# Kernel optimization log

Hardware: AMD Instinct MI355X
Metric: run time of the kernel (lower is better)

The kernel has to match this reference:

```python
import jax, jax.numpy as jnp
import numpy as np
import math

B, S, D = 8, 2048, 1024

def setup_inputs() -> dict:
    key = jax.random.key(0)
    ks = jax.random.split(key, 9)
    scale = 1.0 / math.sqrt(D)
    Q = jax.random.normal(ks[0], (B, S, D), dtype=jnp.float32)
    K = jax.random.normal(ks[1], (B, S, D), dtype=jnp.float32)
    V = jax.random.normal(ks[2], (B, S, D), dtype=jnp.float32)
    Wq = jax.random.normal(ks[3], (D, D), dtype=jnp.float32) * scale
    Wk = jax.random.normal(ks[4], (D, D), dtype=jnp.float32) * scale
    Wv = jax.random.normal(ks[5], (D, D), dtype=jnp.float32) * scale
    bq = jnp.zeros((D,), dtype=jnp.float32)
    bk = jnp.zeros((D,), dtype=jnp.float32)
    bv = jnp.zeros((D,), dtype=jnp.float32)
    # causal mask, broadcast over batch: [1, S, S]
    mask = jnp.tril(jnp.ones((S, S), dtype=jnp.int32))[None, :, :]
    return {"Q": Q, "K": K, "V": V, "Wq": Wq, "Wk": Wk, "Wv": Wv,
            "bq": bq, "bk": bk, "bv": bv, "mask": mask}

def reference(Q, K, V, Wq, Wk, Wv, bq, bk, bv, mask):
    d_model = Q.shape[-1]
    q = jnp.einsum('bsd,de->bse', Q, Wq) + bq
    k = jnp.einsum('bsd,de->bse', K, Wk) + bk
    v = jnp.einsum('bsd,de->bse', V, Wv) + bv
    scores = jnp.einsum('bqd,bkd->bqk', q, k) / math.sqrt(d_model)  # [B,S,S]
    scores = jnp.where(mask == 0, jnp.float32(-1e9), scores)
    weights = jax.nn.softmax(scores, axis=-1)
    out = jnp.einsum('bqk,bkd->bqd', weights, v)
    return out
```

## Files before the change

kernel.cpp:

```cpp
#include <hip/hip_runtime.h>
#include <hip/hip_bf16.h>

#define Bb 8
#define Ss 2048
#define Dd 1024

typedef short bf16x8 __attribute__((ext_vector_type(8)));
typedef float f32x4  __attribute__((ext_vector_type(4)));

__device__ __forceinline__ short f2bf(float f) {
  union { __hip_bfloat16 h; short s; } u;
  u.h = __float2bfloat16(f);
  return u.s;
}
__device__ __forceinline__ float bf2f(short s) {
  union { unsigned int u; float f; } v;
  v.u = ((unsigned int)(unsigned short)s) << 16;
  return v.f;
}

__device__ __forceinline__ int swz(int row, int slot) {
  return row * 64 + (((slot ^ row) & 7) << 3);
}
__device__ __forceinline__ int swzf(int row, int slot) {
  return row * 64 + (((slot ^ row) & 15) << 2);
}

__device__ __forceinline__ void stage_glds(const short* __restrict__ src, int ld,
                                           short* lds, int tid) {
  int w = tid >> 6;
#pragma unroll
  for (int it = 0; it < 4; ++it) {
    int u = it * 256 + tid;
    int r = u >> 3;
    int ssrc = (u ^ r) & 7;
    const short* g = src + (size_t)r * ld + ssrc * 8;
    short* lbase = lds + (size_t)(it * 256 + w * 64) * 8;
    __builtin_amdgcn_global_load_lds((const __attribute__((address_space(1))) void*)g,
                                     (__attribute__((address_space(3))) void*)lbase,
                                     16, 0, 0);
  }
}

__device__ __forceinline__ void stage_glds_f32(const float* __restrict__ src, int ld,
                                               float* lds, int tid) {
  int w = tid >> 6;
#pragma unroll
  for (int it = 0; it < 8; ++it) {
    int u = it * 256 + tid;
    int r = u >> 4;
    int ssrc = (u ^ r) & 15;
    const float* g = src + (size_t)r * ld + ssrc * 4;
    float* lbase = lds + (size_t)(it * 256 + w * 64) * 4;
    __builtin_amdgcn_global_load_lds((const __attribute__((address_space(1))) void*)g,
                                     (__attribute__((address_space(3))) void*)lbase,
                                     16, 0, 0);
  }
}

__device__ __forceinline__ void mfma_tile(const short* ldsA, const short* ldsB,
                                          f32x4 acc[4][4], int wm, int wn, int lr, int lk) {
#pragma unroll
  for (int c = 0; c < 2; ++c) {
    bf16x8 afr[4], bfr[4];
#pragma unroll
    for (int m = 0; m < 4; ++m)
      afr[m] = *(const bf16x8*)&ldsA[swz(wm * 64 + m * 16 + lr, c * 4 + lk)];
#pragma unroll
    for (int n = 0; n < 4; ++n)
      bfr[n] = *(const bf16x8*)&ldsB[swz(wn * 64 + n * 16 + lr, c * 4 + lk)];
#pragma unroll
    for (int m = 0; m < 4; ++m)
#pragma unroll
      for (int n = 0; n < 4; ++n)
        acc[m][n] = __builtin_amdgcn_mfma_f32_16x16x32_bf16(afr[m], bfr[n], acc[m][n], 0, 0, 0);
  }
}

__device__ __forceinline__ void mfma_tile_f32A(const float* ldsA, const short* ldsB,
                                               f32x4 acc[4][4], int wm, int wn,
                                               int lr, int lk) {
#pragma unroll
  for (int c = 0; c < 2; ++c) {
    bf16x8 afr[4], bfr[4];
#pragma unroll
    for (int m = 0; m < 4; ++m) {
      int r = wm * 64 + m * 16 + lr;
      int s0 = c * 8 + lk * 2;
      f32x4 a0 = *(const f32x4*)&ldsA[swzf(r, s0)];
      f32x4 a1 = *(const f32x4*)&ldsA[swzf(r, s0 + 1)];
      bf16x8 h;
      h[0] = f2bf(a0[0]); h[1] = f2bf(a0[1]); h[2] = f2bf(a0[2]); h[3] = f2bf(a0[3]);
      h[4] = f2bf(a1[0]); h[5] = f2bf(a1[1]); h[6] = f2bf(a1[2]); h[7] = f2bf(a1[3]);
      afr[m] = h;
    }
#pragma unroll
    for (int n = 0; n < 4; ++n)
      bfr[n] = *(const bf16x8*)&ldsB[swz(wn * 64 + n * 16 + lr, c * 4 + lk)];
#pragma unroll
    for (int m = 0; m < 4; ++m)
#pragma unroll
      for (int n = 0; n < 4; ++n)
        acc[m][n] = __builtin_amdgcn_mfma_f32_16x16x32_bf16(afr[m], bfr[n], acc[m][n], 0, 0, 0);
  }
}

__global__ void wcast_kernel(const float* __restrict__ Wq, const float* __restrict__ Wk,
                             const float* __restrict__ Wv,
                             short* __restrict__ WtQ, short* __restrict__ WtK,
                             short* __restrict__ WtV) {
  int z = blockIdx.z;
  const float* W = (z == 0) ? Wq : (z == 1) ? Wk : Wv;
  short* Wt      = (z == 0) ? WtQ : (z == 1) ? WtK : WtV;
  __shared__ float tile[32][33];
  int r0 = blockIdx.y * 32, c0 = blockIdx.x * 32;
  int tx = threadIdx.x, ty = threadIdx.y;
#pragma unroll
  for (int ii = 0; ii < 4; ++ii) {
    int r = ty * 4 + ii;
    tile[r][tx] = W[(size_t)(r0 + r) * Dd + c0 + tx];
  }
  __syncthreads();
#pragma unroll
  for (int ii = 0; ii < 4; ++ii) {
    int c = ty * 4 + ii;
    Wt[(size_t)(c0 + c) * Dd + r0 + tx] = f2bf(tile[tx][c]);
  }
}

__launch_bounds__(256, 3)
__global__ void proj_kernel(const float* __restrict__ Q, const float* __restrict__ Kin,
                            const float* __restrict__ V,
                            const short* __restrict__ WtQ, const short* __restrict__ WtK,
                            const short* __restrict__ WtV,
                            const float* __restrict__ bq, const float* __restrict__ bk,
                            const float* __restrict__ bv,
                            short* __restrict__ qb, short* __restrict__ kb,
                            short* __restrict__ vT) {
  __shared__ float ldsA[128 * 64];
  __shared__ short ldsB[128 * 64];
  int z = blockIdx.y;
  const float* A    = (z == 0) ? Q : (z == 1) ? Kin : V;
  const short* W    = (z == 0) ? WtQ : (z == 1) ? WtK : WtV;
  const float* bias = (z == 0) ? bq : (z == 1) ? bk : bv;

  int r = blockIdx.x;
  int x = r & 7;
  int s = r >> 3;
  int nblk = s & 7;
  int mblk = x + 8 * (s >> 3);
  int m0 = mblk * 128;
  int n0 = nblk * 128;

  int tid = threadIdx.x;
  int lane = tid & 63, w = tid >> 6;
  int wm = w >> 1, wn = w & 1;
  int lr = lane & 15, lk = lane >> 4;

  const float* Ab = A + (size_t)m0 * Dd;
  const short* Wb = W + (size_t)n0 * Dd;

  f32x4 acc[4][4] = {};
  for (int k0 = 0; k0 < Dd; k0 += 64) {
    __syncthreads();
    stage_glds_f32(Ab + k0, Dd, ldsA, tid);
    stage_glds(Wb + k0, Dd, ldsB, tid);
    __syncthreads();
    mfma_tile_f32A(ldsA, ldsB, acc, wm, wn, lr, lk);
  }

  if (z < 2) {
    short* out = (z == 0) ? qb : kb;
#pragma unroll
    for (int m = 0; m < 4; ++m)
#pragma unroll
      for (int n = 0; n < 4; ++n) {
        int col = n0 + wn * 64 + n * 16 + lr;
        float bv_ = bias[col];
        int rbase = m0 + wm * 64 + m * 16 + lk * 4;
#pragma unroll
        for (int rr = 0; rr < 4; ++rr)
          out[(size_t)(rbase + rr) * Dd + col] = f2bf(acc[m][n][rr] + bv_);
      }
  } else {
#pragma unroll
    for (int m = 0; m < 4; ++m)
#pragma unroll
      for (int n = 0; n < 4; ++n) {
        int col = n0 + wn * 64 + n * 16 + lr;
        float bv_ = bias[col];
        int rbase = m0 + wm * 64 + m * 16 + lk * 4;
        int bidx = rbase / Ss;
        int s0 = rbase & (Ss - 1);
        short4 h;
        h.x = f2bf(acc[m][n][0] + bv_);
        h.y = f2bf(acc[m][n][1] + bv_);
        h.z = f2bf(acc[m][n][2] + bv_);
        h.w = f2bf(acc[m][n][3] + bv_);
        *(short4*)&vT[(size_t)bidx * Dd * Ss + (size_t)col * Ss + s0] = h;
      }
  }
}

__launch_bounds__(256, 4)
__global__ void score_kernel(const short* __restrict__ qb, const short* __restrict__ kb,
                             short* __restrict__ SP) {
  int d = blockIdx.x;
  int b = d & 7;
  int sidx = d >> 3;
  int i = (int)((sqrtf(8.f * sidx + 1.f) - 1.f) * 0.5f);
  while ((i + 1) * (i + 2) / 2 <= sidx) ++i;
  while (i * (i + 1) / 2 > sidx) --i;
  int j = sidx - i * (i + 1) / 2;

  __shared__ short ldsA[128 * 64];
  __shared__ short ldsB[128 * 64];
  int tid = threadIdx.x;
  int lane = tid & 63, w = tid >> 6;
  int wm = w >> 1, wn = w & 1;
  int lr = lane & 15, lk = lane >> 4;

  const short* Abase = qb + (size_t)b * Ss * Dd + (size_t)i * 128 * Dd;
  const short* Bbase = kb + (size_t)b * Ss * Dd + (size_t)j * 128 * Dd;

  f32x4 acc[4][4] = {};
  for (int k0 = 0; k0 < Dd; k0 += 64) {
    __syncthreads();
    stage_glds(Abase + k0, Dd, ldsA, tid);
    stage_glds(Bbase + k0, Dd, ldsB, tid);
    __syncthreads();
    mfma_tile(ldsA, ldsB, acc, wm, wn, lr, lk);
  }

  short* srow = SP + (size_t)b * Ss * Ss;
#pragma unroll
  for (int m = 0; m < 4; ++m)
#pragma unroll
    for (int n = 0; n < 4; ++n) {
      int colg = j * 128 + wn * 64 + n * 16 + lr;
      int rbase = i * 128 + wm * 64 + m * 16 + lk * 4;
#pragma unroll
      for (int rr = 0; rr < 4; ++rr) {
        int rowg = rbase + rr;
        float sv = acc[m][n][rr] * 0.03125f;
        if (colg > rowg) sv = -1e9f;
        srow[(size_t)rowg * Ss + colg] = f2bf(sv);
      }
    }
}

__global__ void softmax_kernel(short* __restrict__ SP) {
  int row = blockIdx.x;
  int b = row >> 11;
  int q = row & (Ss - 1);
  int L = ((q >> 7) + 1) << 7;
  short* srow = SP + (size_t)b * Ss * Ss + (size_t)q * Ss;
  int tid = threadIdx.x;
  int lane = tid & 63, w = tid >> 6;

  float vals[8];
  int cnt = 0;
  float mx = -3.0e38f;
  for (int c = tid; c < L; c += 256) {
    float f = bf2f(srow[c]);
    vals[cnt++] = f;
    mx = fmaxf(mx, f);
  }
  __shared__ float red[8];
#pragma unroll
  for (int off = 32; off; off >>= 1) mx = fmaxf(mx, __shfl_xor(mx, off));
  if (lane == 0) red[w] = mx;
  __syncthreads();
  mx = fmaxf(fmaxf(red[0], red[1]), fmaxf(red[2], red[3]));

  float sum = 0.f;
  for (int k2 = 0; k2 < cnt; ++k2) {
    float e = __expf(vals[k2] - mx);
    vals[k2] = e;
    sum += e;
  }
#pragma unroll
  for (int off = 32; off; off >>= 1) sum += __shfl_xor(sum, off);
  if (lane == 0) red[4 + w] = sum;
  __syncthreads();
  sum = red[4] + red[5] + red[6] + red[7];
  float inv = 1.0f / sum;

  cnt = 0;
  for (int c = tid; c < L; c += 256) srow[c] = f2bf(vals[cnt++] * inv);
}

__launch_bounds__(256, 4)
__global__ void pv_kernel(const short* __restrict__ SP, const short* __restrict__ vT,
                          float* __restrict__ out) {
  int d = blockIdx.x;
  int b = d & 7;
  int s = d >> 3;
  int i = s >> 3;
  int dblk = s & 7;

  __shared__ short ldsA[128 * 64];
  __shared__ short ldsB[128 * 64];
  int tid = threadIdx.x;
  int lane = tid & 63, w = tid >> 6;
  int wm = w >> 1, wn = w & 1;
  int lr = lane & 15, lk = lane >> 4;

  const short* Abase = SP + (size_t)b * Ss * Ss + (size_t)i * 128 * Ss;
  const short* Bbase = vT + (size_t)b * Dd * Ss + (size_t)dblk * 128 * Ss;
  int KL = (i + 1) * 128;

  f32x4 acc[4][4] = {};
  for (int k0 = 0; k0 < KL; k0 += 64) {
    __syncthreads();
    stage_glds(Abase + k0, Ss, ldsA, tid);
    stage_glds(Bbase + k0, Ss, ldsB, tid);
    __syncthreads();
    mfma_tile(ldsA, ldsB, acc, wm, wn, lr, lk);
  }

#pragma unroll
  for (int m = 0; m < 4; ++m)
#pragma unroll
    for (int n = 0; n < 4; ++n) {
      int colg = dblk * 128 + wn * 64 + n * 16 + lr;
      int rbase = i * 128 + wm * 64 + m * 16 + lk * 4;
#pragma unroll
      for (int rr = 0; rr < 4; ++rr)
        out[(size_t)b * Ss * Dd + (size_t)(rbase + rr) * Dd + colg] = acc[m][n][rr];
    }
}

extern "C" void kernel_launch(void* const* d_in, const int* in_sizes, int n_in,
                              void* d_out, int out_size, void* d_ws, size_t ws_size,
                              hipStream_t stream) {
  const float* Q  = (const float*)d_in[0];
  const float* K  = (const float*)d_in[1];
  const float* V  = (const float*)d_in[2];
  const float* Wq = (const float*)d_in[3];
  const float* Wk = (const float*)d_in[4];
  const float* Wv = (const float*)d_in[5];
  const float* bq = (const float*)d_in[6];
  const float* bk = (const float*)d_in[7];
  const float* bv = (const float*)d_in[8];
  float* out = (float*)d_out;

  char* ws = (char*)d_ws;
  size_t off = 0;
  short* WtQ = (short*)(ws + off); off += (size_t)Dd * Dd * 2;
  short* WtK = (short*)(ws + off); off += (size_t)Dd * Dd * 2;
  short* WtV = (short*)(ws + off); off += (size_t)Dd * Dd * 2;
  short* qb  = (short*)(ws + off); off += (size_t)Bb * Ss * Dd * 2;
  short* kb  = (short*)(ws + off); off += (size_t)Bb * Ss * Dd * 2;
  short* vT  = (short*)(ws + off); off += (size_t)Bb * Ss * Dd * 2;
  short* SP  = (short*)(ws + off); off += (size_t)Bb * Ss * Ss * 2;
  (void)ws_size; (void)in_sizes; (void)n_in; (void)out_size;

  wcast_kernel<<<dim3(32, 32, 3), dim3(32, 8), 0, stream>>>(Wq, Wk, Wv, WtQ, WtK, WtV);
  proj_kernel<<<dim3(1024, 3), 256, 0, stream>>>(Q, K, V, WtQ, WtK, WtV, bq, bk, bv,
                                                 qb, kb, vT);
  score_kernel<<<dim3(1088), 256, 0, stream>>>(qb, kb, SP);
  softmax_kernel<<<dim3(Bb * Ss), 256, 0, stream>>>(SP);
  pv_kernel<<<dim3(1024), 256, 0, stream>>>(SP, vT, out);
}
```

Before: 313.0 us.

## Halve projection K-tile for higher occupancy and vectorize softmax row access

The projection GEMM now stages K-chunks of 32 instead of 64. This shrinks the fp32 A tile and the bf16 B tile in LDS, uses new swizzle layouts, and raises launch bounds from 3 to 6 blocks per CU to increase occupancy. The trade-off is twice as many barrier-separated loop iterations and less MFMA work per sync. The softmax kernel also switches from strided scalar bf16 loads and stores to one 16-byte vector per thread, which reduces memory instructions.

```diff
diff --git a/kernel.cpp b/kernel.cpp
--- a/kernel.cpp
+++ b/kernel.cpp
@@ -22,8 +22,18 @@
 __device__ __forceinline__ int swz(int row, int slot) {
   return row * 64 + (((slot ^ row) & 7) << 3);
 }
-__device__ __forceinline__ int swzf(int row, int slot) {
-  return row * 64 + (((slot ^ row) & 15) << 2);
+__device__ __forceinline__ int swzA32(int row, int slot) {
+  return row * 32 + (((slot ^ row) & 7) << 2);
+}
+__device__ __forceinline__ int swzp(int r, int lk) {
+  int R = r >> 1;
+  int slot = ((r & 1) << 2) | lk;
+  return R * 64 + (((slot ^ R) & 7) << 3);
+}
+
+__device__ __forceinline__ void gld16(const void* g, void* l) {
+  __builtin_amdgcn_global_load_lds((const __attribute__((address_space(1))) void*)g,
+                                   (__attribute__((address_space(3))) void*)l, 16, 0, 0);
 }
 
 __device__ __forceinline__ void stage_glds(const short* __restrict__ src, int ld,
@@ -34,27 +44,34 @@
     int u = it * 256 + tid;
     int r = u >> 3;
     int ssrc = (u ^ r) & 7;
-    const short* g = src + (size_t)r * ld + ssrc * 8;
-    short* lbase = lds + (size_t)(it * 256 + w * 64) * 8;
-    __builtin_amdgcn_global_load_lds((const __attribute__((address_space(1))) void*)g,
-                                     (__attribute__((address_space(3))) void*)lbase,
-                                     16, 0, 0);
-  }
-}
-
-__device__ __forceinline__ void stage_glds_f32(const float* __restrict__ src, int ld,
-                                               float* lds, int tid) {
+    gld16(src + (size_t)r * ld + ssrc * 8, lds + (size_t)(it * 256 + w * 64) * 8);
+  }
+}
+
+__device__ __forceinline__ void stage_A32(const float* __restrict__ src, int ld,
+                                          float* lds, int tid) {
   int w = tid >> 6;
 #pragma unroll
-  for (int it = 0; it < 8; ++it) {
+  for (int it = 0; it < 4; ++it) {
     int u = it * 256 + tid;
-    int r = u >> 4;
-    int ssrc = (u ^ r) & 15;
-    const float* g = src + (size_t)r * ld + ssrc * 4;
-    float* lbase = lds + (size_t)(it * 256 + w * 64) * 4;
-    __builtin_amdgcn_global_load_lds((const __attribute__((address_space(1))) void*)g,
-                                     (__attribute__((address_space(3))) void*)lbase,
-                                     16, 0, 0);
+    int r = u >> 3;
+    int sl = u & 7;
+    int s = sl ^ (r & 7);
+    gld16(src + (size_t)r * ld + s * 4, lds + (size_t)(it * 256 + w * 64) * 4);
+  }
+}
+
+__device__ __forceinline__ void stage_B32(const short* __restrict__ src, int ld,
+                                          short* lds, int tid) {
+  int w = tid >> 6;
+#pragma unroll
+  for (int it = 0; it < 2; ++it) {
+    int u = it * 256 + tid;
+    int R = u >> 3, sl = u & 7;
+    int pre = sl ^ (R & 7);
+    int r = (R << 1) | (pre >> 2);
+    int kc = pre & 3;
+    gld16(src + (size_t)r * ld + kc * 8, lds + (size_t)(it * 256 + w * 64) * 8);
   }
 }
 
@@ -66,34 +83,6 @@
 #pragma unroll
     for (int m = 0; m < 4; ++m)
       afr[m] = *(const bf16x8*)&ldsA[swz(wm * 64 + m * 16 + lr, c * 4 + lk)];
-#pragma unroll
-    for (int n = 0; n < 4; ++n)
-      bfr[n] = *(const bf16x8*)&ldsB[swz(wn * 64 + n * 16 + lr, c * 4 + lk)];
-#pragma unroll
-    for (int m = 0; m < 4; ++m)
-#pragma unroll
-      for (int n = 0; n < 4; ++n)
-        acc[m][n] = __builtin_amdgcn_mfma_f32_16x16x32_bf16(afr[m], bfr[n], acc[m][n], 0, 0, 0);
-  }
-}
-
-__device__ __forceinline__ void mfma_tile_f32A(const float* ldsA, const short* ldsB,
-                                               f32x4 acc[4][4], int wm, int wn,
-                                               int lr, int lk) {
-#pragma unroll
-  for (int c = 0; c < 2; ++c) {
-    bf16x8 afr[4], bfr[4];
-#pragma unroll
-    for (int m = 0; m < 4; ++m) {
-      int r = wm * 64 + m * 16 + lr;
-      int s0 = c * 8 + lk * 2;
-      f32x4 a0 = *(const f32x4*)&ldsA[swzf(r, s0)];
-      f32x4 a1 = *(const f32x4*)&ldsA[swzf(r, s0 + 1)];
-      bf16x8 h;
-      h[0] = f2bf(a0[0]); h[1] = f2bf(a0[1]); h[2] = f2bf(a0[2]); h[3] = f2bf(a0[3]);
-      h[4] = f2bf(a1[0]); h[5] = f2bf(a1[1]); h[6] = f2bf(a1[2]); h[7] = f2bf(a1[3]);
-      afr[m] = h;
-    }
 #pragma unroll
     for (int n = 0; n < 4; ++n)
       bfr[n] = *(const bf16x8*)&ldsB[swz(wn * 64 + n * 16 + lr, c * 4 + lk)];
@@ -128,7 +117,7 @@
   }
 }
 
-__launch_bounds__(256, 3)
+__launch_bounds__(256, 6)
 __global__ void proj_kernel(const float* __restrict__ Q, const float* __restrict__ Kin,
                             const float* __restrict__ V,
                             const short* __restrict__ WtQ, const short* __restrict__ WtK,
@@ -137,8 +126,8 @@
                             const float* __restrict__ bv,
                             short* __restrict__ qb, short* __restrict__ kb,
                             short* __restrict__ vT) {
-  __shared__ float ldsA[128 * 64];
-  __shared__ short ldsB[128 * 64];
+  __shared__ float ldsA[128 * 32];
+  __shared__ short ldsB[64 * 64];
   int z = blockIdx.y;
   const float* A    = (z == 0) ? Q : (z == 1) ? Kin : V;
   const short* W    = (z == 0) ? WtQ : (z == 1) ? WtK : WtV;
@@ -161,12 +150,30 @@
   const short* Wb = W + (size_t)n0 * Dd;
 
   f32x4 acc[4][4] = {};
-  for (int k0 = 0; k0 < Dd; k0 += 64) {
-    __syncthreads();
-    stage_glds_f32(Ab + k0, Dd, ldsA, tid);
-    stage_glds(Wb + k0, Dd, ldsB, tid);
-    __syncthreads();
-    mfma_tile_f32A(ldsA, ldsB, acc, wm, wn, lr, lk);
+  for (int k0 = 0; k0 < Dd; k0 += 32) {
+    __syncthreads();
+    stage_A32(Ab + k0, Dd, ldsA, tid);
+    stage_B32(Wb + k0, Dd, ldsB, tid);
+    __syncthreads();
+    bf16x8 afr[4], bfr[4];
+#pragma unroll
+    for (int m = 0; m < 4; ++m) {
+      int rr = wm * 64 + m * 16 + lr;
+      f32x4 a0 = *(const f32x4*)&ldsA[swzA32(rr, lk * 2)];
+      f32x4 a1 = *(const f32x4*)&ldsA[swzA32(rr, lk * 2 + 1)];
+      bf16x8 h;
+      h[0] = f2bf(a0[0]); h[1] = f2bf(a0[1]); h[2] = f2bf(a0[2]); h[3] = f2bf(a0[3]);
+      h[4] = f2bf(a1[0]); h[5] = f2bf(a1[1]); h[6] = f2bf(a1[2]); h[7] = f2bf(a1[3]);
+      afr[m] = h;
+    }
+#pragma unroll
+    for (int n = 0; n < 4; ++n)
+      bfr[n] = *(const bf16x8*)&ldsB[swzp(wn * 64 + n * 16 + lr, lk)];
+#pragma unroll
+    for (int m = 0; m < 4; ++m)
+#pragma unroll
+      for (int n = 0; n < 4; ++n)
+        acc[m][n] = __builtin_amdgcn_mfma_f32_16x16x32_bf16(afr[m], bfr[n], acc[m][n], 0, 0, 0);
   }
 
   if (z < 2) {
@@ -257,14 +264,18 @@
   short* srow = SP + (size_t)b * Ss * Ss + (size_t)q * Ss;
   int tid = threadIdx.x;
   int lane = tid & 63, w = tid >> 6;
-
-  float vals[8];
-  int cnt = 0;
+  int c8 = tid * 8;
+  bool act = c8 < L;
+
+  float v[8];
   float mx = -3.0e38f;
-  for (int c = tid; c < L; c += 256) {
-    float f = bf2f(srow[c]);
-    vals[cnt++] = f;
-    mx = fmaxf(mx, f);
+  if (act) {
+    bf16x8 hv = *(const bf16x8*)&srow[c8];
+#pragma unroll
+    for (int j2 = 0; j2 < 8; ++j2) {
+      v[j2] = bf2f(hv[j2]);
+      mx = fmaxf(mx, v[j2]);
+    }
   }
   __shared__ float red[8];
 #pragma unroll
@@ -274,10 +285,12 @@
   mx = fmaxf(fmaxf(red[0], red[1]), fmaxf(red[2], red[3]));
 
   float sum = 0.f;
-  for (int k2 = 0; k2 < cnt; ++k2) {
-    float e = __expf(vals[k2] - mx);
-    vals[k2] = e;
-    sum += e;
+  if (act) {
+#pragma unroll
+    for (int j2 = 0; j2 < 8; ++j2) {
+      v[j2] = __expf(v[j2] - mx);
+      sum += v[j2];
+    }
   }
 #pragma unroll
   for (int off = 32; off; off >>= 1) sum += __shfl_xor(sum, off);
@@ -286,8 +299,12 @@
   sum = red[4] + red[5] + red[6] + red[7];
   float inv = 1.0f / sum;
 
-  cnt = 0;
-  for (int c = tid; c < L; c += 256) srow[c] = f2bf(vals[cnt++] * inv);
+  if (act) {
+    bf16x8 ho;
+#pragma unroll
+    for (int j2 = 0; j2 < 8; ++j2) ho[j2] = f2bf(v[j2] * inv);
+    *(bf16x8*)&srow[c8] = ho;
+  }
 }
 
 __launch_bounds__(256, 4)
```

Result: slower. 1.211 ms (+286.7%).
